# Performance work log

Hardware: AMD Instinct MI355X
Metric: run time of the kernel (lower is better)

The kernel has to match this reference:

```python
import jax, jax.numpy as jnp
import numpy as np

D_MODEL = 1024
N_HEADS = 16
HEAD_DIM = D_MODEL // N_HEADS
N_MEM = 16
EPS = 1e-5
ROPE_THETA = 10000.0


def layernorm(x, g, b):
    mu = jnp.mean(x, axis=-1, keepdims=True)
    var = jnp.mean(jnp.square(x - mu), axis=-1, keepdims=True)
    return (x - mu) * jax.lax.rsqrt(var + EPS) * g + b


def rope_cos_sin(seq_len, head_dim, dtype):
    inv_freq = 1.0 / (ROPE_THETA ** (jnp.arange(0, head_dim, 2, dtype=jnp.float32) / head_dim))
    pos = jnp.arange(seq_len, dtype=jnp.float32)
    freqs = pos[:, None] * inv_freq[None, :]            # [S, hd/2]
    emb = jnp.concatenate([freqs, freqs], axis=-1)       # [S, hd]
    return jnp.cos(emb).astype(dtype), jnp.sin(emb).astype(dtype)


def rotate_half(x):
    x1, x2 = jnp.split(x, 2, axis=-1)
    return jnp.concatenate([-x2, x1], axis=-1)


def setup_inputs() -> dict:
    key = jax.random.key(0)
    ks = jax.random.split(key, 8)
    B, T, D = 2, 2048, D_MODEL
    x = jax.random.normal(ks[0], (B, T, D), dtype=jnp.float32)
    memory_tokens = jax.random.normal(ks[1], (1, N_MEM, D), dtype=jnp.float32) * 0.02
    s = 1.0 / np.sqrt(D)
    qkv_w = jax.random.uniform(ks[2], (3 * D, D), minval=-s, maxval=s, dtype=jnp.float32)
    qkv_b = jax.random.uniform(ks[3], (3 * D,), minval=-s, maxval=s, dtype=jnp.float32)
    out_w = jax.random.uniform(ks[4], (D, D), minval=-s, maxval=s, dtype=jnp.float32)
    out_b = jax.random.uniform(ks[5], (D,), minval=-s, maxval=s, dtype=jnp.float32)
    norm_g = jnp.ones((D,), jnp.float32)
    norm_b = jnp.zeros((D,), jnp.float32)
    normm_g = jnp.ones((D,), jnp.float32)
    normm_b = jnp.zeros((D,), jnp.float32)
    return {"x": x, "memory_tokens": memory_tokens, "qkv_w": qkv_w, "qkv_b": qkv_b,
            "out_w": out_w, "out_b": out_b, "norm_g": norm_g, "norm_b": norm_b,
            "normm_g": normm_g, "normm_b": normm_b}


def reference(x, memory_tokens, qkv_w, qkv_b, out_w, out_b, norm_g, norm_b, normm_g, normm_b):
    B, T, D = x.shape
    S = N_MEM + T
    residual = x
    x_norm = layernorm(x, norm_g, norm_b)
    mem = layernorm(jnp.broadcast_to(memory_tokens, (B, N_MEM, D)), normm_g, normm_b)
    xm = jnp.concatenate([mem, x_norm], axis=1)                # [B, S, D]
    qkv = xm @ qkv_w.T + qkv_b                                 # [B, S, 3D]
    qkv = qkv.reshape(B, S, 3, N_HEADS, HEAD_DIM)
    q = jnp.transpose(qkv[:, :, 0], (0, 2, 1, 3))              # [B, H, S, hd]
    k = jnp.transpose(qkv[:, :, 1], (0, 2, 1, 3))
    v = jnp.transpose(qkv[:, :, 2], (0, 2, 1, 3))
    cos, sin = rope_cos_sin(S, HEAD_DIM, x.dtype)              # [S, hd]
    q = q * cos + rotate_half(q) * sin
    k = k * cos + rotate_half(k) * sin
    scale = 1.0 / np.sqrt(HEAD_DIM)
    scores = jnp.einsum("bhqd,bhkd->bhqk", q, k) * scale       # [B, H, S, S]
    causal = jnp.tril(jnp.ones((S, S), dtype=bool))
    scores = jnp.where(causal, scores, jnp.finfo(scores.dtype).min)
    attn = jax.nn.softmax(scores, axis=-1)
    out = jnp.einsum("bhqk,bhkd->bhqd", attn, v)               # [B, H, S, hd]
    out = jnp.transpose(out, (0, 2, 1, 3)).reshape(B, S, D)
    out = out @ out_w.T + out_b
    out = out[:, N_MEM:, :]
    return residual + out
```

## Files before the change

kernel.cpp:

```cpp
#include <hip/hip_runtime.h>
#include <cstdint>


using bf16 = __bf16;
typedef __attribute__((ext_vector_type(8))) __bf16 bf16x8;
typedef __attribute__((ext_vector_type(4))) __bf16 bf16x4;
typedef __attribute__((ext_vector_type(4))) float floatx4;

#define MFMA16(a, b, c) __builtin_amdgcn_mfma_f32_16x16x32_bf16(a, b, c, 0, 0, 0)

constexpr int SV = 2064;
constexpr int SP = 2112;
constexpr float LOG2_THETA = 13.287712379549449f;

__device__ __forceinline__ bool dt_is_bf16(const void* p) {
  return *(const uint32_t*)p == 0x3F803F80u;
}

struct f8 { float v[8]; };

__device__ __forceinline__ f8 load8(const void* p, size_t idx, bool bf) {
  f8 r;
  if (bf) {
    bf16x8 t = *(const bf16x8*)((const bf16*)p + idx);
#pragma unroll
    for (int j = 0; j < 8; ++j) r.v[j] = (float)t[j];
  } else {
    float4 a = *(const float4*)((const float*)p + idx);
    float4 b = *(const float4*)((const float*)p + idx + 4);
    r.v[0] = a.x; r.v[1] = a.y; r.v[2] = a.z; r.v[3] = a.w;
    r.v[4] = b.x; r.v[5] = b.y; r.v[6] = b.z; r.v[7] = b.w;
  }
  return r;
}

__device__ __forceinline__ float ld1(const void* p, size_t idx, bool bf) {
  return bf ? (float)((const bf16*)p)[idx] : ((const float*)p)[idx];
}

__device__ __forceinline__ void load16_to_lds(const bf16* gptr, bf16* lptr) {
  auto* g = reinterpret_cast<const __attribute__((address_space(1))) uint32_t*>(
      reinterpret_cast<uintptr_t>(gptr));
  auto* l = reinterpret_cast<__attribute__((address_space(3))) uint32_t*>(
      reinterpret_cast<uintptr_t>(lptr));
  __builtin_amdgcn_global_load_lds(g, l, 16, 0, 0);
}

__device__ __forceinline__ unsigned cvtpk_bf16(float lo, float hi) {
  unsigned r;
  asm("v_cvt_pk_bf16_f32 %0, %1, %2" : "=v"(r) : "v"(lo), "v"(hi));
  return r;
}

__global__ __launch_bounds__(256) void prep1(
    const void* __restrict__ x, const void* __restrict__ mem,
    const void* __restrict__ ng, const void* __restrict__ nb,
    const void* __restrict__ mg, const void* __restrict__ mb,
    const void* __restrict__ qkvw, bf16* __restrict__ mem16,
    bf16* __restrict__ xln, bf16* __restrict__ Wqb, float2* __restrict__ rtab,
    bf16* __restrict__ Qg, bf16* __restrict__ Kg, bf16* __restrict__ Vg) {
  const int bx = blockIdx.x;
  const int t = threadIdx.x;
  if (bx < 1536) {
    const bool bf = dt_is_bf16(ng);
    const size_t i = ((size_t)bx * 256 + t) * 8;
    const f8 v = load8(qkvw, i, bf);
    bf16x8 o;
#pragma unroll
    for (int j = 0; j < 8; ++j) o[j] = (bf16)v.v[j];
    *(bf16x8*)&Wqb[i] = o;
  } else if (bx < 2564) {
    const bool bf = dt_is_bf16(ng);
    const int wid = t >> 6, lane = t & 63;
    const int row = (bx - 1536) * 4 + wid;
    const void *src, *g, *bb;
    size_t soff;
    bf16* out;
    if (row < 16) {
      src = mem; soff = (size_t)row * 1024; g = mg; bb = mb;
      out = mem16 + (size_t)row * 1024;
    } else {
      src = x; soff = (size_t)(row - 16) * 1024; g = ng; bb = nb;
      out = xln + (size_t)(row - 16) * 1024;
    }
    const f8 v0 = load8(src, soff + lane * 8, bf);
    const f8 v1 = load8(src, soff + 512 + lane * 8, bf);
    float sum = 0.f, sq = 0.f;
#pragma unroll
    for (int j = 0; j < 8; ++j) { sum += v0.v[j]; sq += v0.v[j] * v0.v[j]; }
#pragma unroll
    for (int j = 0; j < 8; ++j) { sum += v1.v[j]; sq += v1.v[j] * v1.v[j]; }
#pragma unroll
    for (int off = 1; off < 64; off <<= 1) {
      sum += __shfl_xor(sum, off);
      sq += __shfl_xor(sq, off);
    }
    const float mu = sum * (1.0f / 1024.0f);
    const float var = sq * (1.0f / 1024.0f) - mu * mu;
    const float rstd = rsqrtf(var + 1e-5f);
    const f8 g0 = load8(g, lane * 8, bf), g1 = load8(g, 512 + lane * 8, bf);
    const f8 b0 = load8(bb, lane * 8, bf), b1 = load8(bb, 512 + lane * 8, bf);
    bf16x8 o0, o1;
#pragma unroll
    for (int j = 0; j < 8; ++j) {
      o0[j] = (bf16)((v0.v[j] - mu) * rstd * g0.v[j] + b0.v[j]);
      o1[j] = (bf16)((v1.v[j] - mu) * rstd * g1.v[j] + b1.v[j]);
    }
    *(bf16x8*)&out[lane * 8] = o0;
    *(bf16x8*)&out[512 + lane * 8] = o1;
  } else if (bx < 2822) {
    const int i = (bx - 2564) * 256 + t;
    const int pos = i >> 5, f = i & 31;
    const float ang = (float)pos * exp2f((float)f * (-LOG2_THETA / 32.0f));
    float c, s;
    sincosf(ang, &c, &s);
    rtab[i] = make_float2(c, s);
  } else {
    const int bz = bx - 2822;
    const int bh = bz / 3;
    const int arr = bz % 3;
    const bf16x8 z{};
    if (arr < 2) {
      bf16* base = (arr == 0 ? Qg : Kg) + ((size_t)bh * SP + SV) * 64;
      for (int j = t; j < 384; j += 256) *(bf16x8*)&base[j * 8] = z;
    } else {
      for (int j = t; j < 384; j += 256) {
        const int d = j / 6, c = (j % 6) * 8;
        *(bf16x8*)&Vg[((size_t)bh * 64 + d) * SP + SV + c] = z;
      }
    }
  }
}

__global__ __launch_bounds__(512, 1) void gemm0_rope(
    const bf16* __restrict__ mem16, const bf16* __restrict__ xln,
    const bf16* __restrict__ Wqb, const void* __restrict__ bias,
    const void* __restrict__ flagp, const float2* __restrict__ rtab,
    bf16* __restrict__ Qg, bf16* __restrict__ Kg, bf16* __restrict__ Vg) {
  const bool bf = dt_is_bf16(flagp);
  __shared__ bf16 SH[65536];
  const int t = threadIdx.x;
  const int row0 = blockIdx.x * 256;
  const int col0 = blockIdx.y * 256;
  const int wid = t >> 6, lane = t & 63, lr = lane & 15, lg = lane >> 4;
  const int wm = wid >> 2, wn = wid & 3;
  const int xorv = (lr & 7) << 3;

  const int coff = (((t & 7) ^ ((t >> 3) & 7)) << 3);
  const bf16* aptr[4];
  const bf16* bptr[4];
#pragma unroll
  for (int s = 0; s < 4; ++s) {
    int g = row0 + s * 64 + (t >> 3);
    if (g > 4127) g = 4127;
    const int b2 = (g >= SV) ? 1 : 0;
    const int ss = g - b2 * SV;
    const bf16* ap = (ss < 16) ? (mem16 + (size_t)ss * 1024)
                               : (xln + ((size_t)(b2 * 2048 + ss - 16)) * 1024);
    aptr[s] = ap + coff;
    bptr[s] = Wqb + (size_t)(col0 + s * 64 + (t >> 3)) * 1024 + coff;
  }

  const int ldsbase = (t & ~63) * 8;
  auto STAGE = [&](int bufi, int k0) {
    bf16* Ld = SH + bufi * 32768;
#pragma unroll
    for (int s = 0; s < 4; ++s)
      load16_to_lds(aptr[s] + k0, Ld + s * 4096 + ldsbase);
#pragma unroll
    for (int s = 0; s < 4; ++s)
      load16_to_lds(bptr[s] + k0, Ld + 16384 + s * 4096 + ldsbase);
  };

  floatx4 acc[8][4] = {};
  STAGE(0, 0);
  STAGE(1, 64);

  for (int kt = 0; kt < 16; ++kt) {
    const int cur = kt & 1;
    if (kt < 15)
      asm volatile("s_waitcnt vmcnt(8)" ::: "memory");
    else
      asm volatile("s_waitcnt vmcnt(0)" ::: "memory");
    __builtin_amdgcn_s_barrier();
    __builtin_amdgcn_sched_barrier(0);
    const bf16* Ab = SH + cur * 32768;
    const bf16* Bb = Ab + 16384;
    bf16x8 a0[8], b0[4], a1[8], b1[4];
#pragma unroll
    for (int mi = 0; mi < 8; ++mi)
      a0[mi] = *(const bf16x8*)&Ab[(wm * 128 + mi * 16 + lr) * 64 + ((lg * 8) ^ xorv)];
#pragma unroll
    for (int ni = 0; ni < 4; ++ni)
      b0[ni] = *(const bf16x8*)&Bb[(wn * 64 + ni * 16 + lr) * 64 + ((lg * 8) ^ xorv)];
    __builtin_amdgcn_s_setprio(1);
#pragma unroll
    for (int mi = 0; mi < 8; ++mi)
#pragma unroll
      for (int ni = 0; ni < 4; ++ni)
        acc[mi][ni] = MFMA16(a0[mi], b0[ni], acc[mi][ni]);
    __builtin_amdgcn_s_setprio(0);
#pragma unroll
    for (int mi = 0; mi < 8; ++mi)
      a1[mi] = *(const bf16x8*)&Ab[(wm * 128 + mi * 16 + lr) * 64 + ((32 + lg * 8) ^ xorv)];
#pragma unroll
    for (int ni = 0; ni < 4; ++ni)
      b1[ni] = *(const bf16x8*)&Bb[(wn * 64 + ni * 16 + lr) * 64 + ((32 + lg * 8) ^ xorv)];
    __builtin_amdgcn_sched_barrier(0);
    asm volatile("s_waitcnt lgkmcnt(0)" ::: "memory");
    __builtin_amdgcn_s_barrier();
    __builtin_amdgcn_sched_barrier(0);
    if (kt < 14) STAGE(cur, (kt + 2) * 64);
    __builtin_amdgcn_s_setprio(1);
#pragma unroll
    for (int mi = 0; mi < 8; ++mi)
#pragma unroll
      for (int ni = 0; ni < 4; ++ni)
        acc[mi][ni] = MFMA16(a1[mi], b1[ni], acc[mi][ni]);
    __builtin_amdgcn_s_setprio(0);
  }

  const int colbase = col0 + wn * 64;
  const int part = colbase >> 10;
  const int h = (colbase >> 6) & 15;
  const int row0w = row0 + wm * 128;

  if (part == 2) {
#pragma unroll
    for (int mi = 0; mi < 8; ++mi) {
      const int gq = row0w + mi * 16 + lg * 4;
      if (gq >= 2 * SV) continue;
      const int b2 = (gq >= SV) ? 1 : 0;
      const int pos = gq - b2 * SV;
      const size_t hb = (size_t)(b2 * 16 + h) * 64;
#pragma unroll
      for (int ni = 0; ni < 4; ++ni) {
        const int d = ni * 16 + lr;
        const float bc = ld1(bias, colbase + ni * 16 + lr, bf);
        bf16x4 vv;
#pragma unroll
        for (int r = 0; r < 4; ++r) vv[r] = (bf16)(acc[mi][ni][r] + bc);
        *(bf16x4*)&Vg[(hb + d) * SP + pos] = vv;
      }
    }
  } else {
    bf16* Dst = (part == 0) ? Qg : Kg;
    const float qs = (part == 0) ? 0.18033688011f : 1.0f;
    float bv[4];
#pragma unroll
    for (int a = 0; a < 4; ++a) bv[a] = ld1(bias, colbase + a * 16 + lr, bf);
#pragma unroll
    for (int mi = 0; mi < 8; ++mi) {
#pragma unroll
      for (int r = 0; r < 4; ++r) {
        const int g = row0w + mi * 16 + lg * 4 + r;
        if (g >= 2 * SV) continue;
        const int b2 = (g >= SV) ? 1 : 0;
        const int pos = g - b2 * SV;
        bf16* drow = Dst + ((size_t)(b2 * 16 + h) * SP + pos) * 64;
#pragma unroll
        for (int a = 0; a < 2; ++a) {
          const float2 cs = rtab[pos * 32 + a * 16 + lr];
          const float vlo = (acc[mi][a][r] + bv[a]) * qs;
          const float vhi = (acc[mi][a + 2][r] + bv[a + 2]) * qs;
          drow[a * 16 + lr] = (bf16)(vlo * cs.x - vhi * cs.y);
          drow[32 + a * 16 + lr] = (bf16)(vhi * cs.x + vlo * cs.y);
        }
      }
    }
  }
}

__global__ __launch_bounds__(256) void flash3f(
    const bf16* __restrict__ Qg, const bf16* __restrict__ Kg,
    const bf16* __restrict__ Vg, const void* __restrict__ Wo,
    const void* __restrict__ flagp, bf16* __restrict__ Wob,
    bf16* __restrict__ attn_out) {
  if (blockIdx.x >= 33) {
    const int cid = (blockIdx.x - 33) * 32 + blockIdx.y;
    const bool bf = dt_is_bf16(flagp);
    const size_t i = ((size_t)cid * 256 + threadIdx.x) * 8;
    const f8 v = load8(Wo, i, bf);
    bf16x8 o;
#pragma unroll
    for (int j = 0; j < 8; ++j) o[j] = (bf16)v.v[j];
    *(bf16x8*)&Wob[i] = o;
    return;
  }
  const int qt = 32 - blockIdx.x;
  const int bh = blockIdx.y;
  const int b = bh >> 4, h = bh & 15;
  const bf16* Qb = Qg + (size_t)bh * SP * 64;
  const bf16* Kb = Kg + (size_t)bh * SP * 64;
  const bf16* Vb = Vg + (size_t)bh * 64 * SP;

  const int t = threadIdx.x;
  const int wid = t >> 6, lane = t & 63, lr = lane & 15, lg = lane >> 4;
  const int qw0 = qt * 64 + wid * 16;
  const int q = qw0 + lr;

  __shared__ bf16 Ks[2][64 * 72];
  __shared__ bf16 Vt[2][64 * 64];

  bf16x8 qf0{}, qf1{};
  if (q < SV) {
    qf0 = *(const bf16x8*)&Qb[(size_t)q * 64 + lg * 8];
    qf1 = *(const bf16x8*)&Qb[(size_t)q * 64 + 32 + lg * 8];
  }

  floatx4 o[4] = {};
  float lsum = 0.f;

  const int kr = t >> 2;
  const int kc = (t & 3) * 16;
  const int vd = t >> 2;
  const int vg0 = t & 3;
  const int vswz = ((vd & 7) ^ ((vd >> 4) & 3)) << 3;

  bf16x8 kA, kB, vA, vB;
  kA = *(const bf16x8*)&Kb[(size_t)kr * 64 + kc];
  kB = *(const bf16x8*)&Kb[(size_t)kr * 64 + kc + 8];
  vA = *(const bf16x8*)&Vb[(size_t)vd * SP + vg0 * 8];
  vB = *(const bf16x8*)&Vb[(size_t)vd * SP + (vg0 + 4) * 8];

  *(bf16x8*)&Ks[0][kr * 72 + kc] = kA;
  *(bf16x8*)&Ks[0][kr * 72 + kc + 8] = kB;
  *(bf16x8*)&Vt[0][vd * 64 + ((vg0 << 3) ^ vswz)] = vA;
  *(bf16x8*)&Vt[0][vd * 64 + (((vg0 + 4) << 3) ^ vswz)] = vB;
  if (qt >= 1) {
    kA = *(const bf16x8*)&Kb[(size_t)(64 + kr) * 64 + kc];
    kB = *(const bf16x8*)&Kb[(size_t)(64 + kr) * 64 + kc + 8];
    vA = *(const bf16x8*)&Vb[(size_t)vd * SP + 64 + vg0 * 8];
    vB = *(const bf16x8*)&Vb[(size_t)vd * SP + 64 + (vg0 + 4) * 8];
  }
  asm volatile("s_waitcnt lgkmcnt(0)" ::: "memory");
  __builtin_amdgcn_s_barrier();
  __builtin_amdgcn_sched_barrier(0);

  for (int kt = 0; kt <= qt; ++kt) {
    const int cur = kt & 1;
    const int k0 = kt * 64;
    if (kt < qt) {
      const int nb2 = cur ^ 1;
      *(bf16x8*)&Ks[nb2][kr * 72 + kc] = kA;
      *(bf16x8*)&Ks[nb2][kr * 72 + kc + 8] = kB;
      *(bf16x8*)&Vt[nb2][vd * 64 + ((vg0 << 3) ^ vswz)] = vA;
      *(bf16x8*)&Vt[nb2][vd * 64 + (((vg0 + 4) << 3) ^ vswz)] = vB;
      if (kt + 1 < qt) {
        const int kn = k0 + 128;
        kA = *(const bf16x8*)&Kb[(size_t)(kn + kr) * 64 + kc];
        kB = *(const bf16x8*)&Kb[(size_t)(kn + kr) * 64 + kc + 8];
        vA = *(const bf16x8*)&Vb[(size_t)vd * SP + kn + vg0 * 8];
        vB = *(const bf16x8*)&Vb[(size_t)vd * SP + kn + (vg0 + 4) * 8];
      }
    }

    floatx4 c[4] = {};
    __builtin_amdgcn_s_setprio(1);
#pragma unroll
    for (int j2 = 0; j2 < 4; ++j2) {
      const bf16x8 kfa = *(const bf16x8*)&Ks[cur][(j2 * 16 + lr) * 72 + lg * 8];
      const bf16x8 kfb = *(const bf16x8*)&Ks[cur][(j2 * 16 + lr) * 72 + 32 + lg * 8];
      c[j2] = MFMA16(kfa, qf0, c[j2]);
      c[j2] = MFMA16(kfb, qf1, c[j2]);
    }
    __builtin_amdgcn_s_setprio(0);

    const bool nm = (k0 + 63 > qw0);
    float pr[4][4];
#pragma unroll
    for (int j2 = 0; j2 < 4; ++j2) {
#pragma unroll
      for (int rr = 0; rr < 4; ++rr) {
        float s = c[j2][rr];
        if (nm && (k0 + j2 * 16 + lg * 4 + rr > q)) s = -1e30f;
        float p;
        asm("v_exp_f32 %0, %1" : "=v"(p) : "v"(s));
        lsum += p;
        pr[j2][rr] = p;
      }
    }

    unsigned paw[2][4];
#pragma unroll
    for (int cc = 0; cc < 2; ++cc) {
#pragma unroll
      for (int p_ = 0; p_ < 2; ++p_) {
        unsigned a = cvtpk_bf16(pr[2 * cc][2 * p_], pr[2 * cc][2 * p_ + 1]);
        unsigned b2 = cvtpk_bf16(pr[2 * cc + 1][2 * p_], pr[2 * cc + 1][2 * p_ + 1]);
        asm("v_permlane32_swap_b32 %0, %1" : "+v"(a), "+v"(b2));
        asm("v_permlane16_swap_b32 %0, %1" : "+v"(a), "+v"(b2));
        paw[cc][p_] = a;
        paw[cc][2 + p_] = b2;
      }
    }

    __builtin_amdgcn_s_setprio(1);
#pragma unroll
    for (int cc = 0; cc < 2; ++cc) {
      union { unsigned w[4]; bf16x8 v; } pu;
      pu.w[0] = paw[cc][0]; pu.w[1] = paw[cc][1];
      pu.w[2] = paw[cc][2]; pu.w[3] = paw[cc][3];
#pragma unroll
      for (int dt = 0; dt < 4; ++dt) {
        const int key8 = (cc * 32 + lg * 8) ^ ((((lr & 7) ^ dt)) << 3);
        const bf16x8 vf = *(const bf16x8*)&Vt[cur][(dt * 16 + lr) * 64 + key8];
        o[dt] = MFMA16(pu.v, vf, o[dt]);
      }
    }
    __builtin_amdgcn_s_setprio(0);
    asm volatile("s_waitcnt lgkmcnt(0)" ::: "memory");
    __builtin_amdgcn_s_barrier();
    __builtin_amdgcn_sched_barrier(0);
  }

  float l = lsum;
  l += __shfl_xor(l, 16);
  l += __shfl_xor(l, 32);
#pragma unroll
  for (int r = 0; r < 4; ++r) {
    const float lv = __shfl(l, lg * 4 + r);
    const int s = qw0 + lg * 4 + r;
    if (s < 16 || s >= SV) continue;
    const float inv = 1.0f / lv;
    const size_t rowoff = ((size_t)(b * 2048 + s - 16)) * 1024 + h * 64;
#pragma unroll
    for (int dt = 0; dt < 4; ++dt)
      attn_out[rowoff + dt * 16 + lr] = (bf16)(o[dt][r] * inv);
  }
}

__global__ __launch_bounds__(512, 1) void gemm1_proj(
    const bf16* __restrict__ A, const bf16* __restrict__ Wob,
    const void* __restrict__ bias, const void* __restrict__ x,
    const void* __restrict__ flagp, void* __restrict__ outp) {
  const bool bf = dt_is_bf16(flagp);
  __shared__ bf16 SH[32768];
  const int t = threadIdx.x;
  const int row0 = blockIdx.x * 128;
  const int col0 = blockIdx.y * 128;
  const int wid = t >> 6, lane = t & 63, lr = lane & 15, lg = lane >> 4;
  const int wm = wid >> 2, wn = wid & 3;
  const int xorv = (lr & 7) << 3;

  const int coff = (((t & 7) ^ ((t >> 3) & 7)) << 3);
  const bf16* aptr[2];
  const bf16* bptr[2];
#pragma unroll
  for (int s = 0; s < 2; ++s) {
    aptr[s] = A + (size_t)(row0 + s * 64 + (t >> 3)) * 1024 + coff;
    bptr[s] = Wob + (size_t)(col0 + s * 64 + (t >> 3)) * 1024 + coff;
  }
  const int ldsbase = (t & ~63) * 8;
  auto STAGE = [&](int bufi, int k0) {
    bf16* Ld = SH + bufi * 16384;
#pragma unroll
    for (int s = 0; s < 2; ++s)
      load16_to_lds(aptr[s] + k0, Ld + s * 4096 + ldsbase);
#pragma unroll
    for (int s = 0; s < 2; ++s)
      load16_to_lds(bptr[s] + k0, Ld + 8192 + s * 4096 + ldsbase);
  };

  floatx4 acc[4][2] = {};
  STAGE(0, 0);
  STAGE(1, 64);

  for (int kt = 0; kt < 16; ++kt) {
    const int cur = kt & 1;
    if (kt < 15)
      asm volatile("s_waitcnt vmcnt(4)" ::: "memory");
    else
      asm volatile("s_waitcnt vmcnt(0)" ::: "memory");
    __builtin_amdgcn_s_barrier();
    __builtin_amdgcn_sched_barrier(0);
    const bf16* Ab = SH + cur * 16384;
    const bf16* Bb = Ab + 8192;
    bf16x8 a0[4], b0[2], a1[4], b1[2];
#pragma unroll
    for (int mi = 0; mi < 4; ++mi)
      a0[mi] = *(const bf16x8*)&Ab[(wm * 64 + mi * 16 + lr) * 64 + ((lg * 8) ^ xorv)];
#pragma unroll
    for (int ni = 0; ni < 2; ++ni)
      b0[ni] = *(const bf16x8*)&Bb[(wn * 32 + ni * 16 + lr) * 64 + ((lg * 8) ^ xorv)];
    __builtin_amdgcn_s_setprio(1);
#pragma unroll
    for (int mi = 0; mi < 4; ++mi)
#pragma unroll
      for (int ni = 0; ni < 2; ++ni)
        acc[mi][ni] = MFMA16(a0[mi], b0[ni], acc[mi][ni]);
    __builtin_amdgcn_s_setprio(0);
#pragma unroll
    for (int mi = 0; mi < 4; ++mi)
      a1[mi] = *(const bf16x8*)&Ab[(wm * 64 + mi * 16 + lr) * 64 + ((32 + lg * 8) ^ xorv)];
#pragma unroll
    for (int ni = 0; ni < 2; ++ni)
      b1[ni] = *(const bf16x8*)&Bb[(wn * 32 + ni * 16 + lr) * 64 + ((32 + lg * 8) ^ xorv)];
    __builtin_amdgcn_sched_barrier(0);
    asm volatile("s_waitcnt lgkmcnt(0)" ::: "memory");
    __builtin_amdgcn_s_barrier();
    __builtin_amdgcn_sched_barrier(0);
    if (kt < 14) STAGE(cur, (kt + 2) * 64);
    __builtin_amdgcn_s_setprio(1);
#pragma unroll
    for (int mi = 0; mi < 4; ++mi)
#pragma unroll
      for (int ni = 0; ni < 2; ++ni)
        acc[mi][ni] = MFMA16(a1[mi], b1[ni], acc[mi][ni]);
    __builtin_amdgcn_s_setprio(0);
  }

#pragma unroll
  for (int mi = 0; mi < 4; ++mi) {
#pragma unroll
    for (int r = 0; r < 4; ++r) {
      const int row = row0 + wm * 64 + mi * 16 + lg * 4 + r;
#pragma unroll
      for (int ni = 0; ni < 2; ++ni) {
        const int col = col0 + wn * 32 + ni * 16 + lr;
        const size_t idx = (size_t)row * 1024 + col;
        const float v = acc[mi][ni][r] + ld1(bias, col, bf) + ld1(x, idx, bf);
        if (bf)
          ((bf16*)outp)[idx] = (bf16)v;
        else
          ((float*)outp)[idx] = v;
      }
    }
  }
}

extern "C" void kernel_launch(void* const* d_in, const int* in_sizes, int n_in,
                              void* d_out, int out_size, void* d_ws, size_t ws_size,
                              hipStream_t stream) {
  const void* x = d_in[0];
  const void* mem = d_in[1];
  const void* qkvw = d_in[2];
  const void* qkvb = d_in[3];
  const void* outw = d_in[4];
  const void* outb = d_in[5];
  const void* ng = d_in[6];
  const void* nb = d_in[7];
  const void* mg = d_in[8];
  const void* mb = d_in[9];

  char* ws = (char*)d_ws;
  bf16* mem16 = (bf16*)(ws);
  bf16* xln = (bf16*)(ws + 32768);
  bf16* Qg = (bf16*)(ws + 8421376);
  bf16* Kg = (bf16*)(ws + 17072128);
  bf16* Vg = (bf16*)(ws + 25722880);
  bf16* Wqb = (bf16*)(ws + 34373632);
  bf16* Wob = (bf16*)(ws + 40665088);
  bf16* attn = xln;
  float2* rtab = (float2*)Wob;

  prep1<<<2918, 256, 0, stream>>>(x, mem, ng, nb, mg, mb, qkvw,
                                  mem16, xln, Wqb, rtab, Qg, Kg, Vg);
  gemm0_rope<<<dim3(17, 12), 512, 0, stream>>>(mem16, xln, Wqb, qkvb, ng, rtab,
                                               Qg, Kg, Vg);
  flash3f<<<dim3(49, 32), 256, 0, stream>>>(Qg, Kg, Vg, outw, ng, Wob, attn);
  gemm1_proj<<<dim3(32, 8), 512, 0, stream>>>(attn, Wob, outb, x, ng, d_out);
}
```

Before: 204.6 us.

## Split GEMM k-step into four phases and reorder flash grid launch

The QKV GEMM inner loop is restructured into four phases, each loading half the A fragments and issuing 16 MFMAs. The global-to-LDS staging for the next tile is split across phases to interleave memory traffic with compute. The barriers per k-step change, which may add sync overhead. Separately, the flash attention grid is transposed so that the Wo conversion blocks come last along y with a guard on the block id, changing block dispatch order so heavy causal tiles are issued first.

```diff
diff --git a/kernel.cpp b/kernel.cpp
--- a/kernel.cpp
+++ b/kernel.cpp
@@ -162,7 +162,7 @@
   }
 
   const int ldsbase = (t & ~63) * 8;
-  auto STAGE = [&](int bufi, int k0) {
+  auto STAGE_ALL = [&](int bufi, int k0) {
     bf16* Ld = SH + bufi * 32768;
 #pragma unroll
     for (int s = 0; s < 4; ++s)
@@ -173,51 +173,64 @@
   };
 
   floatx4 acc[8][4] = {};
-  STAGE(0, 0);
-  STAGE(1, 64);
+  STAGE_ALL(0, 0);
+  STAGE_ALL(1, 64);
 
   for (int kt = 0; kt < 16; ++kt) {
     const int cur = kt & 1;
+    const bf16* Ab = SH + cur * 32768;
+    const bf16* Bb = Ab + 16384;
+    bf16* Ld = SH + cur * 32768;
+    const int k2 = (kt + 2) * 64;
+    const bool st = (kt <= 13);
+
     if (kt < 15)
       asm volatile("s_waitcnt vmcnt(8)" ::: "memory");
     else
       asm volatile("s_waitcnt vmcnt(0)" ::: "memory");
     __builtin_amdgcn_s_barrier();
     __builtin_amdgcn_sched_barrier(0);
-    const bf16* Ab = SH + cur * 32768;
-    const bf16* Bb = Ab + 16384;
-    bf16x8 a0[8], b0[4], a1[8], b1[4];
-#pragma unroll
-    for (int mi = 0; mi < 8; ++mi)
-      a0[mi] = *(const bf16x8*)&Ab[(wm * 128 + mi * 16 + lr) * 64 + ((lg * 8) ^ xorv)];
-#pragma unroll
-    for (int ni = 0; ni < 4; ++ni)
-      b0[ni] = *(const bf16x8*)&Bb[(wn * 64 + ni * 16 + lr) * 64 + ((lg * 8) ^ xorv)];
-    __builtin_amdgcn_s_setprio(1);
-#pragma unroll
-    for (int mi = 0; mi < 8; ++mi)
-#pragma unroll
-      for (int ni = 0; ni < 4; ++ni)
-        acc[mi][ni] = MFMA16(a0[mi], b0[ni], acc[mi][ni]);
-    __builtin_amdgcn_s_setprio(0);
-#pragma unroll
-    for (int mi = 0; mi < 8; ++mi)
-      a1[mi] = *(const bf16x8*)&Ab[(wm * 128 + mi * 16 + lr) * 64 + ((32 + lg * 8) ^ xorv)];
-#pragma unroll
-    for (int ni = 0; ni < 4; ++ni)
-      b1[ni] = *(const bf16x8*)&Bb[(wn * 64 + ni * 16 + lr) * 64 + ((32 + lg * 8) ^ xorv)];
-    __builtin_amdgcn_sched_barrier(0);
-    asm volatile("s_waitcnt lgkmcnt(0)" ::: "memory");
-    __builtin_amdgcn_s_barrier();
-    __builtin_amdgcn_sched_barrier(0);
-    if (kt < 14) STAGE(cur, (kt + 2) * 64);
-    __builtin_amdgcn_s_setprio(1);
-#pragma unroll
-    for (int mi = 0; mi < 8; ++mi)
-#pragma unroll
-      for (int ni = 0; ni < 4; ++ni)
-        acc[mi][ni] = MFMA16(a1[mi], b1[ni], acc[mi][ni]);
-    __builtin_amdgcn_s_setprio(0);
+
+    bf16x8 af[4], bfr[4];
+#pragma unroll
+    for (int ph = 0; ph < 4; ++ph) {
+      const int mh = ph & 1;
+      const int ks = ph >> 1;
+      const int kcol = (ks * 32 + lg * 8) ^ xorv;
+#pragma unroll
+      for (int mi = 0; mi < 4; ++mi)
+        af[mi] = *(const bf16x8*)&Ab[(wm * 128 + mh * 64 + mi * 16 + lr) * 64 + kcol];
+      if (mh == 0) {
+#pragma unroll
+        for (int ni = 0; ni < 4; ++ni)
+          bfr[ni] = *(const bf16x8*)&Bb[(wn * 64 + ni * 16 + lr) * 64 + kcol];
+      }
+      if (ph == 3 && st) {
+        load16_to_lds(aptr[0] + k2, Ld + 0 * 4096 + ldsbase);
+        load16_to_lds(aptr[2] + k2, Ld + 2 * 4096 + ldsbase);
+#pragma unroll
+        for (int s = 0; s < 4; ++s)
+          load16_to_lds(bptr[s] + k2, Ld + 16384 + s * 4096 + ldsbase);
+      }
+      __builtin_amdgcn_s_barrier();
+      asm volatile("s_waitcnt lgkmcnt(0)" ::: "memory");
+      __builtin_amdgcn_sched_barrier(0);
+      __builtin_amdgcn_s_setprio(1);
+#pragma unroll
+      for (int mi = 0; mi < 4; ++mi)
+#pragma unroll
+        for (int ni = 0; ni < 4; ++ni)
+          acc[mh * 4 + mi][ni] = MFMA16(af[mi], bfr[ni], acc[mh * 4 + mi][ni]);
+      __builtin_amdgcn_s_setprio(0);
+      if (ph >= 2) {
+        __builtin_amdgcn_s_barrier();
+        __builtin_amdgcn_sched_barrier(0);
+      }
+    }
+    if (st) {
+      load16_to_lds(aptr[1] + k2, Ld + 1 * 4096 + ldsbase);
+      load16_to_lds(aptr[3] + k2, Ld + 3 * 4096 + ldsbase);
+    }
   }
 
   const int colbase = col0 + wn * 64;
@@ -276,8 +289,9 @@
     const bf16* __restrict__ Vg, const void* __restrict__ Wo,
     const void* __restrict__ flagp, bf16* __restrict__ Wob,
     bf16* __restrict__ attn_out) {
-  if (blockIdx.x >= 33) {
-    const int cid = (blockIdx.x - 33) * 32 + blockIdx.y;
+  if (blockIdx.y >= 32) {
+    const int cid = (blockIdx.y - 32) * 33 + blockIdx.x;
+    if (cid >= 512) return;
     const bool bf = dt_is_bf16(flagp);
     const size_t i = ((size_t)cid * 256 + threadIdx.x) * 8;
     const f8 v = load8(Wo, i, bf);
@@ -558,6 +572,6 @@
                                   mem16, xln, Wqb, rtab, Qg, Kg, Vg);
   gemm0_rope<<<dim3(17, 12), 512, 0, stream>>>(mem16, xln, Wqb, qkvb, ng, rtab,
                                                Qg, Kg, Vg);
-  flash3f<<<dim3(49, 32), 256, 0, stream>>>(Qg, Kg, Vg, outw, ng, Wob, attn);
+  flash3f<<<dim3(33, 48), 256, 0, stream>>>(Qg, Kg, Vg, outw, ng, Wob, attn);
   gemm1_proj<<<dim3(32, 8), 512, 0, stream>>>(attn, Wob, outb, x, ng, d_out);
 }
```

After: 199.8 us. 1.02x faster.
